# Kernel optimization log

Hardware: AMD Instinct MI355X
Metric: run time of the kernel (lower is better)

The kernel has to match this reference:

```python
import jax, jax.numpy as jnp
import numpy as np
from jax import lax

B = 100000      # number of time steps (outer 'batch' loop in the torch code)
SEQ = 1         # inner seq_len
SPIN = 365      # spinLen
TRAIN = 50000   # traintimeLen


def setup_inputs() -> dict:
    key = jax.random.key(0)
    k1, k2, k3, k4, k5 = jax.random.split(key, 5)
    x = jax.random.uniform(k1, (B, SEQ, 2), dtype=jnp.float32)          # [batch, seq, 2] (batch_first)
    y_obs = jax.random.uniform(k2, (B, 1), dtype=jnp.float32)
    weight_r_yom = jax.random.uniform(k3, (1, 1), dtype=jnp.float32)
    weight_r_ylm = jax.random.uniform(k4, (1, 1), dtype=jnp.float32)
    weight_r_yfm = jax.random.uniform(k5, (1, 1), dtype=jnp.float32)
    return {"x": x, "y_obs": y_obs, "weight_r_yom": weight_r_yom,
            "weight_r_ylm": weight_r_ylm, "weight_r_yfm": weight_r_yfm,
            "epoch": 0, "time_lag": 0}


def reference(x, y_obs, weight_r_yom, weight_r_ylm, weight_r_yfm, epoch, time_lag):
    batch_size = x.shape[0]
    dtype = x.dtype
    # obs std over training window (torch.std is unbiased -> ddof=1)
    obsstd = jnp.std(y_obs[SPIN:TRAIN], ddof=1)

    # gates from softmax over the three scalar weights (constant over time)
    ew = jnp.exp(jnp.stack([weight_r_yom, weight_r_ylm, weight_r_yfm]))  # [3,1,1]
    denom = ew.sum(0)
    oo = ew[0] / denom   # (1,1) outflow gate
    ol = ew[1] / denom   # (1,1) loss (ET) gate

    def time_step(c0, u):
        # c0: (1,1) cell state; u: (2,) = (precip u1, PET u2)
        u1, u2 = u[0], u[1]
        safe_c = jnp.where(c0 > 0, c0, jnp.asarray(1.0, dtype))
        olc_raw = jnp.where(c0 > 0, ol - jax.nn.elu(ol - u2 / safe_c), ol)
        f = jax.nn.relu(1.0 - oo - olc_raw)          # forget gate uses pre-relu constraint
        olc = jax.nn.relu(olc_raw)
        c1 = f * c0 + u1                              # ib = 0 -> full input
        outs = (oo * c0, c0, ol * c0, olc * c0, olc, f)
        return c1, outs

    def batch_step(c0, u_seq):
        # u_seq: [SEQ, 2]; stored outputs correspond to the LAST inner t step
        c1, outs = lax.scan(time_step, c0, u_seq)
        return c1, tuple(o[-1] for o in outs)

    c_init = jnp.zeros((1, 1), dtype=dtype)
    _, (q, c, l, lc, g_olc, g_f) = lax.scan(batch_step, c_init, x[time_lag:])

    def pad(a):
        a = a.reshape(-1, 1)
        return jnp.concatenate([jnp.zeros((time_lag, 1), dtype), a], axis=0)

    h_n = pad(q)                     # bp = ib*g = 0, so h_n == q_n == oo*c0
    c_n = pad(c)
    l_n = pad(l)
    lc_n = pad(lc)
    Gate_olc = pad(g_olc)
    Gate_f = pad(g_f)

    tail = jnp.concatenate([jnp.zeros((time_lag, 1), dtype),
                            jnp.ones((batch_size - time_lag, 1), dtype)], axis=0)
    Gate_oo = oo[0, 0] * tail
    Gate_ol = ol[0, 0] * tail
    obs_std = obsstd * tail

    zeros = jnp.zeros((batch_size, 1), dtype)
    bp_n = zeros
    Gate_ib = zeros
    h_nout = jnp.concatenate([h_n, obs_std], axis=1)

    return (h_n, c_n, l_n, lc_n, bp_n, Gate_ib, Gate_oo, Gate_ol,
            Gate_olc, Gate_f, h_nout, obs_std)
```

## Files before the change

kernel.cpp:

```cpp
#include <hip/hip_runtime.h>
#include <math.h>

#define NB      100000
#define TRAIN   50000
#define SPIN    365
#define CHUNK_L 21
#define WARM    64
#define SCAN_TPB 256
#define NCHUNK   ((NB + CHUNK_L - 1) / CHUNK_L)
#define SCAN_BLKS ((NCHUNK + SCAN_TPB - 1) / SCAN_TPB)
#define WIN_MAX  (SCAN_TPB * CHUNK_L + WARM)

#define RED_BLOCKS 64
#define RED_TPB    256
#define V4_BASE  368
#define V4_COUNT 12408


struct ShMain {
    union {
        float2 win[WIN_MAX + 8];
        struct { double ssum[RED_TPB]; double ssq[RED_TPB]; } red;
    } u;
};

__global__ __launch_bounds__(256) void k_main(const float* __restrict__ x,
                                              const float* __restrict__ y_obs,
                                              const float* __restrict__ w0,
                                              const float* __restrict__ w1,
                                              const float* __restrict__ w2,
                                              float* __restrict__ ws,
                                              float* __restrict__ out) {
    __shared__ ShMain sh;
    int tid = threadIdx.x;

    if (blockIdx.x < SCAN_BLKS) {
        float e0 = expf(w0[0]);
        float e1 = expf(w1[0]);
        float e2 = expf(w2[0]);
        float denom = e0 + e1 + e2;
        const float oo = e0 / denom;
        const float ol = e1 / denom;
        const float omoo = 1.0f - oo;

        int bchunk0 = blockIdx.x * SCAN_TPB;
        int bstart  = bchunk0 * CHUNK_L;
        int r0      = max(0, bstart - WARM);
        int r1      = min(NB, bstart + SCAN_TPB * CHUNK_L);
        int cnt     = r1 - r0;

        {
            const float4* x4 = (const float4*)(((const float2*)x) + r0);
            float4* s4 = (float4*)sh.u.win;
            int n4 = cnt >> 1;
            for (int i = tid; i < n4; i += SCAN_TPB) s4[i] = x4[i];
        }
        __syncthreads();

        int chunk = bchunk0 + tid;
        if (chunk >= NCHUNK) return;

        int s0     = chunk * CHUNK_L;
        int send   = min(s0 + CHUNK_L, NB);
        int wstart = max(0, s0 - WARM);

        float c = (wstart == 0) ? 0.0f : 1.0f;

        const int base = -r0;
        float2 uv = sh.u.win[wstart + base];

        for (int t = wstart; t < s0; ++t) {
            float2 nv = sh.u.win[t + 1 + base];
            float u1 = uv.x, u2 = uv.y;
            float r  = __builtin_amdgcn_rcpf(c);
            float z  = ol - u2 * r;
            float el = (z > 0.0f) ? z : (__expf(z) - 1.0f);
            float praw    = ol - el;
            float olc_raw = (c > 0.0f) ? praw : ol;
            float f  = fmaxf(omoo - olc_raw, 0.0f);
            c = fmaf(f, c, u1);
            uv = nv;
        }

        float* __restrict__ c_n  = out + 1 * NB;
        float* __restrict__ traw = out + 8 * NB;

        for (int t = s0; t < send; ++t) {
            float2 nv = sh.u.win[t + 1 + base];
            float u1 = uv.x, u2 = uv.y;
            float r  = __builtin_amdgcn_rcpf(c);
            float z  = ol - u2 * r;
            float el = (z > 0.0f) ? z : (__expf(z) - 1.0f);
            float praw    = ol - el;
            float olc_raw = (c > 0.0f) ? praw : ol;
            float f  = fmaxf(omoo - olc_raw, 0.0f);

            c_n[t]  = c;
            traw[t] = olc_raw;

            c = fmaf(f, c, u1);
            uv = nv;
        }
    } else {
        int b   = blockIdx.x - SCAN_BLKS;
        int gid = b * RED_TPB + tid;
        double s = 0.0, q = 0.0;
        const float4* y4 = (const float4*)(y_obs + V4_BASE);
        for (int i = gid; i < V4_COUNT; i += RED_BLOCKS * RED_TPB) {
            float4 v = y4[i];
            s += (double)v.x + (double)v.y + (double)v.z + (double)v.w;
            q += (double)v.x * v.x + (double)v.y * v.y
               + (double)v.z * v.z + (double)v.w * v.w;
        }
        if (b == 0 && tid == 0) {
            for (int i = SPIN; i < V4_BASE; ++i) {
                double v = (double)y_obs[i];
                s += v; q += v * v;
            }
        }
        sh.u.red.ssum[tid] = s;
        sh.u.red.ssq[tid]  = q;
        __syncthreads();
        for (int off = RED_TPB / 2; off > 0; off >>= 1) {
            if (tid < off) {
                sh.u.red.ssum[tid] += sh.u.red.ssum[tid + off];
                sh.u.red.ssq[tid]  += sh.u.red.ssq[tid + off];
            }
            __syncthreads();
        }
        if (tid == 0) {
            double* wsd = (double*)(ws + 4);
            wsd[2 * b]     = sh.u.red.ssum[0];
            wsd[2 * b + 1] = sh.u.red.ssq[0];
        }
    }
}

__global__ __launch_bounds__(256) void k_fill(const float* __restrict__ w0,
                                              const float* __restrict__ w1,
                                              const float* __restrict__ w2,
                                              const float* __restrict__ ws,
                                              float* __restrict__ out) {
    __shared__ float sh3[3];
    int tid = threadIdx.x;
    if (tid < 64) {
        const double* wsd = (const double*)(ws + 4);
        double s = wsd[2 * tid];
        double q = wsd[2 * tid + 1];
        for (int off = 32; off > 0; off >>= 1) {
            s += __shfl_down(s, off, 64);
            q += __shfl_down(q, off, 64);
        }
        if (tid == 0) {
            double n    = (double)(TRAIN - SPIN);
            double mean = s / n;
            double var  = (q - n * mean * mean) / (n - 1.0);
            sh3[2] = (float)sqrt(var);
            float e0 = expf(w0[0]);
            float e1 = expf(w1[0]);
            float e2 = expf(w2[0]);
            float denom = e0 + e1 + e2;
            sh3[0] = e0 / denom;
            sh3[1] = e1 / denom;
        }
    }
    __syncthreads();
    float oo = sh3[0], ol = sh3[1], stdv = sh3[2];

    int i = blockIdx.x * 256 + tid;
    if (i >= NB) return;

    float c    = out[1 * NB + i];
    float praw = out[8 * NB + i];
    float olc  = fmaxf(praw, 0.0f);
    float f    = fmaxf(1.0f - oo - praw, 0.0f);
    float h    = oo * c;

    out[0  * NB + i] = h;
    out[2  * NB + i] = ol * c;
    out[3  * NB + i] = olc * c;
    out[4  * NB + i] = 0.0f;
    out[5  * NB + i] = 0.0f;
    out[6  * NB + i] = oo;
    out[7  * NB + i] = ol;
    out[8  * NB + i] = olc;
    out[9  * NB + i] = f;
    float2 hv; hv.x = h; hv.y = stdv;
    ((float2*)(out + 10 * NB))[i] = hv;
    out[12 * NB + i] = stdv;
}

extern "C" void kernel_launch(void* const* d_in, const int* in_sizes, int n_in,
                              void* d_out, int out_size, void* d_ws, size_t ws_size,
                              hipStream_t stream) {
    const float* x     = (const float*)d_in[0];
    const float* y_obs = (const float*)d_in[1];
    const float* w0    = (const float*)d_in[2];
    const float* w1    = (const float*)d_in[3];
    const float* w2    = (const float*)d_in[4];
    float* out = (float*)d_out;
    float* ws  = (float*)d_ws;

    k_main<<<SCAN_BLKS + RED_BLOCKS, 256, 0, stream>>>(x, y_obs, w0, w1, w2, ws, out);
    k_fill<<<(NB + 255) / 256, 256, 0, stream>>>(w0, w1, w2, ws, out);
}
```

Before: 80.77 us.

## Fuse output epilogue into scan kernel with shared-memory transpose for coalesced stores

Each scan thread now keeps its chunk's cell states and raw gate values in register arrays. These are transposed through shared memory, reusing the input window storage. The block then computes and writes the ten per-step outputs with coalesced stores. The fill kernel is reduced to writing the std-dependent outputs, reading only h back. This replaces the stride-21 scattered stores and removes the fill kernel's round trip through global memory, at the cost of extra registers, two more barriers and a fully unrolled inner loop.

```diff
diff --git a/kernel.cpp b/kernel.cpp
--- a/kernel.cpp
+++ b/kernel.cpp
@@ -9,7 +9,8 @@
 #define SCAN_TPB 256
 #define NCHUNK   ((NB + CHUNK_L - 1) / CHUNK_L)
 #define SCAN_BLKS ((NCHUNK + SCAN_TPB - 1) / SCAN_TPB)
-#define WIN_MAX  (SCAN_TPB * CHUNK_L + WARM)
+#define BLK_T    (SCAN_TPB * CHUNK_L)
+#define WIN_MAX  (BLK_T + WARM)
 
 #define RED_BLOCKS 64
 #define RED_TPB    256
@@ -20,6 +21,7 @@
 struct ShMain {
     union {
         float2 win[WIN_MAX + 8];
+        struct { float c[BLK_T]; float p[BLK_T]; } tr;
         struct { double ssum[RED_TPB]; double ssq[RED_TPB]; } red;
     } u;
 };
@@ -46,7 +48,7 @@
         int bchunk0 = blockIdx.x * SCAN_TPB;
         int bstart  = bchunk0 * CHUNK_L;
         int r0      = max(0, bstart - WARM);
-        int r1      = min(NB, bstart + SCAN_TPB * CHUNK_L);
+        int r1      = min(NB, bstart + BLK_T);
         int cnt     = r1 - r0;
 
         {
@@ -57,49 +59,68 @@
         }
         __syncthreads();
 
-        int chunk = bchunk0 + tid;
-        if (chunk >= NCHUNK) return;
-
-        int s0     = chunk * CHUNK_L;
-        int send   = min(s0 + CHUNK_L, NB);
-        int wstart = max(0, s0 - WARM);
-
-        float c = (wstart == 0) ? 0.0f : 1.0f;
-
-        const int base = -r0;
-        float2 uv = sh.u.win[wstart + base];
-
-        for (int t = wstart; t < s0; ++t) {
-            float2 nv = sh.u.win[t + 1 + base];
-            float u1 = uv.x, u2 = uv.y;
-            float r  = __builtin_amdgcn_rcpf(c);
-            float z  = ol - u2 * r;
-            float el = (z > 0.0f) ? z : (__expf(z) - 1.0f);
-            float praw    = ol - el;
-            float olc_raw = (c > 0.0f) ? praw : ol;
-            float f  = fmaxf(omoo - olc_raw, 0.0f);
-            c = fmaf(f, c, u1);
-            uv = nv;
-        }
-
-        float* __restrict__ c_n  = out + 1 * NB;
-        float* __restrict__ traw = out + 8 * NB;
-
-        for (int t = s0; t < send; ++t) {
-            float2 nv = sh.u.win[t + 1 + base];
-            float u1 = uv.x, u2 = uv.y;
-            float r  = __builtin_amdgcn_rcpf(c);
-            float z  = ol - u2 * r;
-            float el = (z > 0.0f) ? z : (__expf(z) - 1.0f);
-            float praw    = ol - el;
-            float olc_raw = (c > 0.0f) ? praw : ol;
-            float f  = fmaxf(omoo - olc_raw, 0.0f);
-
-            c_n[t]  = c;
-            traw[t] = olc_raw;
-
-            c = fmaf(f, c, u1);
-            uv = nv;
+        int   chunk  = bchunk0 + tid;
+        float c_arr[CHUNK_L];
+        float p_arr[CHUNK_L];
+        {
+            int s0     = chunk * CHUNK_L;
+            int wstart = max(0, s0 - WARM);
+            float c = (wstart == 0) ? 0.0f : 1.0f;
+            const int base = -r0;
+
+            for (int t = wstart; t < s0; ++t) {
+                float2 uv = sh.u.win[t + base];
+                float u1 = uv.x, u2 = uv.y;
+                float r  = __builtin_amdgcn_rcpf(c);
+                float z  = ol - u2 * r;
+                float el = (z > 0.0f) ? z : (__expf(z) - 1.0f);
+                float praw    = ol - el;
+                float olc_raw = (c > 0.0f) ? praw : ol;
+                float f  = fmaxf(omoo - olc_raw, 0.0f);
+                c = fmaf(f, c, u1);
+            }
+
+            #pragma unroll
+            for (int j = 0; j < CHUNK_L; ++j) {
+                float2 uv = sh.u.win[s0 + j + base];
+                float u1 = uv.x, u2 = uv.y;
+                float r  = __builtin_amdgcn_rcpf(c);
+                float z  = ol - u2 * r;
+                float el = (z > 0.0f) ? z : (__expf(z) - 1.0f);
+                float praw    = ol - el;
+                float olc_raw = (c > 0.0f) ? praw : ol;
+                float f  = fmaxf(omoo - olc_raw, 0.0f);
+                c_arr[j] = c;
+                p_arr[j] = olc_raw;
+                c = fmaf(f, c, u1);
+            }
+        }
+        __syncthreads();
+
+        #pragma unroll
+        for (int j = 0; j < CHUNK_L; ++j) {
+            sh.u.tr.c[tid * CHUNK_L + j] = c_arr[j];
+            sh.u.tr.p[tid * CHUNK_L + j] = p_arr[j];
+        }
+        __syncthreads();
+
+        int blk_cnt = r1 - bstart;
+        float* __restrict__ o0 = out + bstart;
+        for (int i = tid; i < blk_cnt; i += SCAN_TPB) {
+            float cc   = sh.u.tr.c[i];
+            float praw = sh.u.tr.p[i];
+            float olc  = fmaxf(praw, 0.0f);
+            float f    = fmaxf(omoo - praw, 0.0f);
+            o0[0 * NB + i] = oo * cc;
+            o0[1 * NB + i] = cc;
+            o0[2 * NB + i] = ol * cc;
+            o0[3 * NB + i] = olc * cc;
+            o0[4 * NB + i] = 0.0f;
+            o0[5 * NB + i] = 0.0f;
+            o0[6 * NB + i] = oo;
+            o0[7 * NB + i] = ol;
+            o0[8 * NB + i] = olc;
+            o0[9 * NB + i] = f;
         }
     } else {
         int b   = blockIdx.x - SCAN_BLKS;
@@ -136,12 +157,9 @@
     }
 }
 
-__global__ __launch_bounds__(256) void k_fill(const float* __restrict__ w0,
-                                              const float* __restrict__ w1,
-                                              const float* __restrict__ w2,
-                                              const float* __restrict__ ws,
+__global__ __launch_bounds__(256) void k_fill(const float* __restrict__ ws,
                                               float* __restrict__ out) {
-    __shared__ float sh3[3];
+    __shared__ float shs;
     int tid = threadIdx.x;
     if (tid < 64) {
         const double* wsd = (const double*)(ws + 4);
@@ -155,36 +173,15 @@
             double n    = (double)(TRAIN - SPIN);
             double mean = s / n;
             double var  = (q - n * mean * mean) / (n - 1.0);
-            sh3[2] = (float)sqrt(var);
-            float e0 = expf(w0[0]);
-            float e1 = expf(w1[0]);
-            float e2 = expf(w2[0]);
-            float denom = e0 + e1 + e2;
-            sh3[0] = e0 / denom;
-            sh3[1] = e1 / denom;
+            shs = (float)sqrt(var);
         }
     }
     __syncthreads();
-    float oo = sh3[0], ol = sh3[1], stdv = sh3[2];
+    float stdv = shs;
 
     int i = blockIdx.x * 256 + tid;
     if (i >= NB) return;
-
-    float c    = out[1 * NB + i];
-    float praw = out[8 * NB + i];
-    float olc  = fmaxf(praw, 0.0f);
-    float f    = fmaxf(1.0f - oo - praw, 0.0f);
-    float h    = oo * c;
-
-    out[0  * NB + i] = h;
-    out[2  * NB + i] = ol * c;
-    out[3  * NB + i] = olc * c;
-    out[4  * NB + i] = 0.0f;
-    out[5  * NB + i] = 0.0f;
-    out[6  * NB + i] = oo;
-    out[7  * NB + i] = ol;
-    out[8  * NB + i] = olc;
-    out[9  * NB + i] = f;
+    float h = out[i];
     float2 hv; hv.x = h; hv.y = stdv;
     ((float2*)(out + 10 * NB))[i] = hv;
     out[12 * NB + i] = stdv;
@@ -202,5 +199,5 @@
     float* ws  = (float*)d_ws;
 
     k_main<<<SCAN_BLKS + RED_BLOCKS, 256, 0, stream>>>(x, y_obs, w0, w1, w2, ws, out);
-    k_fill<<<(NB + 255) / 256, 256, 0, stream>>>(w0, w1, w2, ws, out);
+    k_fill<<<(NB + 255) / 256, 256, 0, stream>>>(ws, out);
 }
```

Result: faster. 79.00 us (-2.2%).
